# Performance work log

Measured on AMD Instinct MI355X. Metric: run time of the kernel, lower is better.

The kernel has to match this reference:

```python
import jax, jax.numpy as jnp
import numpy as np
from jax import lax

G = 64      # ngroup
CPN = 4     # channels per group in hidden layers
H, W = 32, 64
K = 5       # conv kernel
BIN = 8     # bin_num
BIAS = 3.5  # (bin_num-1)/2
NMIX = 3    # GMM components (batch replicas)
SCALE = 65536.0


def _group_mask(cout, cin, strict):
    # wavefront causality: tap (dg, di, dj) allowed iff dg+di+dj < 0 (strict) or <= 0
    g = jnp.arange(G)
    dg = g[None, :] - g[:, None]                      # (Gout, Gin)
    off = jnp.arange(K) - K // 2
    dd = off[:, None] + off[None, :]                  # (K, K)
    tot = dg[:, :, None, None] + dd[None, None, :, :]
    m = (tot < 0) if strict else (tot <= 0)
    m = jnp.repeat(jnp.repeat(m, cout, axis=0), cin, axis=1)
    return m.astype(jnp.float32)                      # (G*cout, G*cin, K, K)


def _cconv(x, w, b, m, relu):
    y = lax.conv_general_dilated(x, w * m, (1, 1), 'SAME',
                                 dimension_numbers=('NCHW', 'OIHW', 'NCHW'))
    y = y + b[None, :, None, None]
    return jax.nn.relu(y) if relu else y


def setup_inputs() -> dict:
    key = jax.random.key(0)
    ks = jax.random.split(key, 8)
    data = jax.random.randint(ks[0], (1, G, H, W), 0, BIN).astype(jnp.float32)
    mask = jax.random.randint(ks[1], (1, G, H, W), 0, 2).astype(jnp.float32)
    s = 0.05
    w_in = jax.random.normal(ks[2], (G * CPN, G, K, K), jnp.float32) * s
    b_in = jnp.zeros((G * CPN,), jnp.float32)
    w_hid = jax.random.normal(ks[3], (10, G * CPN, G * CPN, K, K), jnp.float32) * s
    b_hid = jnp.zeros((10, G * CPN), jnp.float32)
    w_out = jax.random.normal(ks[4], (G * NMIX, G * CPN, K, K), jnp.float32) * s
    b_out = jnp.zeros((G * NMIX,), jnp.float32)
    return dict(data=data, mask=mask, w_in=w_in, b_in=b_in,
                w_hid=w_hid, b_hid=b_hid, w_out=w_out, b_out=b_out)


def reference(data, mask, w_in, b_in, w_hid, b_hid, w_out, b_out):
    m_in = _group_mask(CPN, 1, True)      # first layer: strict (excludes current group)
    m_hid = _group_mask(CPN, CPN, False)
    m_out = _group_mask(NMIX, CPN, False)
    tdata = (data - BIAS) * mask
    x = jnp.concatenate([tdata, tdata, tdata], axis=0)   # (3, G, H, W)
    x = _cconv(x, w_in, b_in, m_in, True)
    for i in range(5):                                   # 5 residual blocks
        h = _cconv(x, w_hid[2 * i], b_hid[2 * i], m_hid, True)
        h = _cconv(h, w_hid[2 * i + 1], b_hid[2 * i + 1], m_hid, True)
        x = x + h
    y = _cconv(x, w_out, b_out, m_out, False)            # (3, G*3, H, W)
    y = y.reshape(NMIX, G, NMIX, H, W)                   # batch replica m -> mixture m
    logits = y[:, :, 0]
    mu = y[:, :, 1]
    sig = jax.nn.softplus(y[:, :, 2]) + 1e-6
    wts = jax.nn.softmax(logits, axis=0)                 # (3, G, H, W)
    edges = jnp.arange(BIN, dtype=jnp.float32) + 0.5 - BIAS
    z = (edges[:, None, None, None, None] - mu[None]) / (sig[None] * jnp.float32(np.sqrt(2.0)))
    cdf = 0.5 * (1.0 + lax.erf(z))                       # (BIN, 3, G, H, W)
    table = jnp.einsum('kmghw,mghw->ghwk', cdf, wts) * SCALE
    return table                                         # (G, H, W, BIN) quantizable CDF
```

## Files before the change

### kernel.cpp

```cpp
#include <hip/hip_runtime.h>
#include <math.h>

typedef _Float16 f16;
typedef _Float16 f16x8 __attribute__((ext_vector_type(8)));
typedef float f32x4 __attribute__((ext_vector_type(4)));

#define HH 32
#define WW 64
#define NPX 2048
#define SLOTS 68
#define LOSCALE 2048.0f
#define INV_LOSCALE 4.8828125e-4f

typedef const __attribute__((address_space(1))) void gvoid;
typedef __attribute__((address_space(3))) void lvoid;
__device__ __forceinline__ void gload_lds16(const void* g, void* l) {
    __builtin_amdgcn_global_load_lds((gvoid*)g, (lvoid*)l, 16, 0, 0);
}

__global__ void zero_kernel(f16* p, int n8) {
    int i = blockIdx.x * 256 + threadIdx.x;
    if (i < n8) *(int4*)(p + i * 8) = make_int4(0, 0, 0, 0);
}

__global__ void prep_kernel(const float* __restrict__ data,
                            const float* __restrict__ mask,
                            f16* __restrict__ X0, int plane) {
    int idx = blockIdx.x * 256 + threadIdx.x;
    if (idx >= NPX * 64) return;
    int px = idx >> 6, ci = idx & 63;
    int hh = px >> 6, w = px & 63;
    float v = (data[ci * NPX + px] - 3.5f) * mask[ci * NPX + px];
    int dst = ((hh + 2) * SLOTS + (w + 2)) * 64 + ci;
    X0[dst] = (f16)v;
    X0[plane + dst] = (f16)0.f;
}

__global__ void repack_kernel(const float* __restrict__ W, f16* __restrict__ WP,
                              int cin_log2, int coutp_log2,
                              int cpg_in_log2, int limb, int is_out) {
    int idx = blockIdx.x * 256 + threadIdx.x;
    int Cin = 1 << cin_log2;
    int plane = 25 << (cin_log2 + coutp_log2);
    int ci = idx & (Cin - 1);
    int rest = idx >> cin_log2;
    int co_p = rest & ((1 << coutp_log2) - 1);
    int tap = rest >> coutp_log2;
    if (tap >= 25) return;
    int ky = tap / 5, kx = tap - 5 * ky;
    int co_orig, g_out;
    if (is_out) { g_out = co_p >> 1; co_orig = 3 * g_out + 1 + (co_p & 1); }
    else        { g_out = co_p >> 2; co_orig = co_p; }
    int g_in = ci >> cpg_in_log2;
    float v = 0.f;
    if (ky + kx <= limb + g_out - g_in)
        v = W[(co_orig * Cin + ci) * 25 + tap];
    f16 vh = (f16)v;
    WP[idx] = vh;
    WP[plane + idx] = (f16)((v - (float)vh) * LOSCALE);
}

__global__ __launch_bounds__(320, 3) void conv_kernel(
    const f16* __restrict__ IN, int Cin, int inPlane,
    const f16* __restrict__ WP, int wPlane,
    const float* __restrict__ bias,
    const f16* __restrict__ RES, int resPlane,
    f16* __restrict__ OA, int oaPlane,
    float* __restrict__ OT,
    int nmt, int Coutp, int cpg_out, int cpg_in, int limb, int mode)
{
    __shared__ __align__(16) char SMEM[46080];
    f16* BL = (f16*)SMEM;
    float* RED = (float*)SMEM;

    const int t = threadIdx.x;
    const int kw = t >> 6;
    const int lane = t & 63, l15 = lane & 15, q = lane >> 4;

    int b = blockIdx.x;
    int half = nmt << 4;
    int slot = b >= half ? 1 : 0;
    int idx = b - (slot ? half : 0);
    int mt8 = idx >> 5;
    const int h = idx & 31;
    const int mt = slot ? (nmt - 1 - mt8) : mt8;
    const int co0 = mt * 16;
    const int g_max = (co0 + 15) / cpg_out;

    int cnt[5];
#pragma unroll
    for (int kx = 0; kx < 5; kx++) {
        int c = (g_max + limb - (kw + kx) + 1) * cpg_in;
        c = c < Cin ? c : Cin;
        cnt[kx] = c > 0 ? c : 0;
    }
    int ci_top = (g_max + limb + 1) * cpg_in;
    ci_top = ci_top < Cin ? ci_top : Cin;

    const f16* src[9];
#pragma unroll
    for (int r = 0; r < 9; r++) {
        int u = r * 320 + t;
        if (u >= 2720) u = 0;
        int plane = u / 1360;
        int rem = u - plane * 1360;
        int s4 = rem >> 2;
        int ci16 = rem & 3;
        int row = s4 / 68;
        int slt = s4 - row * 68;
        src[r] = IN + plane * inPlane + ((h + row) * SLOTS + slt) * Cin + ci16 * 8;
    }

    f32x4 acc_h[4], acc_m[4];
#pragma unroll
    for (int j = 0; j < 4; j++) {
        acc_h[j] = (f32x4){0.f, 0.f, 0.f, 0.f};
        acc_m[j] = (f32x4){0.f, 0.f, 0.f, 0.f};
    }

    const size_t kxs = (size_t)Coutp * Cin;

    for (int ci0 = 0; ci0 < ci_top; ci0 += 32) {
        __syncthreads();
#pragma unroll
        for (int r = 0; r < 9; r++) {
            int ub = r * 320 + kw * 64;
            if (ub < 2720)
                gload_lds16(src[r] + ci0, BL + ub * 8);
        }
        __syncthreads();

        const f16* wbase = WP + ((size_t)(kw * 5) * Coutp + co0) * Cin + ci0;
        f16x8 cah, cal, nah, nal;
        if (ci0 < cnt[0]) {
            cah = *(const f16x8*)(wbase + l15 * Cin + q * 8);
            cal = *(const f16x8*)(wbase + wPlane + l15 * Cin + q * 8);
        }
#pragma unroll
        for (int kx = 0; kx < 5; kx++) {
            if (ci0 >= cnt[kx]) break;
            if (kx < 4 && ci0 < cnt[kx + 1]) {
                nah = *(const f16x8*)(wbase + (kx + 1) * kxs + l15 * Cin + q * 8);
                nal = *(const f16x8*)(wbase + (kx + 1) * kxs + wPlane + l15 * Cin + q * 8);
            }
            f16x8 bh[4], bl[4];
#pragma unroll
            for (int j = 0; j < 4; j++) {
                int slt = j * 16 + l15 + kx;
                bh[j] = *(const f16x8*)&BL[(0 * 5 + kw) * (SLOTS * 32) + slt * 32 + q * 8];
                bl[j] = *(const f16x8*)&BL[(1 * 5 + kw) * (SLOTS * 32) + slt * 32 + q * 8];
            }
#pragma unroll
            for (int j = 0; j < 4; j++) {
                acc_h[j] = __builtin_amdgcn_mfma_f32_16x16x32_f16(cah, bh[j], acc_h[j], 0, 0, 0);
                acc_m[j] = __builtin_amdgcn_mfma_f32_16x16x32_f16(cah, bl[j], acc_m[j], 0, 0, 0);
                acc_m[j] = __builtin_amdgcn_mfma_f32_16x16x32_f16(cal, bh[j], acc_m[j], 0, 0, 0);
            }
            cah = nah; cal = nal;
        }
    }

    __syncthreads();
#pragma unroll
    for (int j = 0; j < 4; j++) {
        f32x4 v;
#pragma unroll
        for (int r = 0; r < 4; r++)
            v[r] = acc_h[j][r] + acc_m[j][r] * INV_LOSCALE;
        *(f32x4*)&RED[(kw * 64 + j * 16 + l15) * 20 + q * 4] = v;
    }
    __syncthreads();

    if (mode == 0) {
        for (int c = t; c < 1024; c += 320) {
            int px = c >> 4, col = c & 15;
            float v = bias[co0 + col];
#pragma unroll
            for (int k5 = 0; k5 < 5; k5++) v += RED[(k5 * 64 + px) * 20 + col];
            v = fmaxf(v, 0.f);
            int o = ((h + 2) * SLOTS + px + 2) * Coutp + co0 + col;
            if (RES) v += (float)RES[o] + (float)RES[resPlane + o] * INV_LOSCALE;
            f16 vh = (f16)v;
            OA[o] = vh;
            OA[oaPlane + o] = (f16)((v - (float)vh) * LOSCALE);
        }
    } else {
        for (int c = t; c < 1024; c += 320) {
            int px = c >> 4, col = c & 15;
            float v = bias[3 * ((co0 + col) >> 1) + 1 + (col & 1)];
#pragma unroll
            for (int k5 = 0; k5 < 5; k5++) v += RED[(k5 * 64 + px) * 20 + col];
            RED[px * 20 + col] = v;
        }
        __syncthreads();
        for (int c = t; c < 512; c += 320) {
            int px = c >> 3, gl = c & 7;
            float mu = RED[px * 20 + 2 * gl];
            float s  = RED[px * 20 + 2 * gl + 1];
            float sp = fmaxf(s, 0.f) + log1pf(expf(-fabsf(s)));
            float sig = sp + 1e-6f;
            float inv = 1.f / (sig * 1.41421356237f);
            int g = (co0 >> 1) + gl;
            float* o = OT + ((size_t)g * NPX + h * WW + px) * 8;
#pragma unroll
            for (int k = 0; k < 8; k++) {
                float z = ((float)k - 3.0f - mu) * inv;
                o[k] = 32768.f * (1.f + erff(z));
            }
        }
    }
}

extern "C" void kernel_launch(void* const* d_in, const int* in_sizes, int n_in,
                              void* d_out, int out_size, void* d_ws, size_t ws_size,
                              hipStream_t stream) {
    const float* data  = (const float*)d_in[0];
    const float* mask  = (const float*)d_in[1];
    const float* w_in  = (const float*)d_in[2];
    const float* b_in  = (const float*)d_in[3];
    const float* w_hid = (const float*)d_in[4];
    const float* b_hid = (const float*)d_in[5];
    const float* w_out = (const float*)d_in[6];
    const float* b_out = (const float*)d_in[7];
    float* out = (float*)d_out;

    f16* WP = (f16*)d_ws;
    f16* P  = WP + 3276800;
    f16* Q  = P + 1253376;
    f16* X0 = Q + 1253376;

    zero_kernel<<<1377, 256, 0, stream>>>(P, 352512);
    prep_kernel<<<512, 256, 0, stream>>>(data, mask, X0, 156672);

    repack_kernel<<<1600, 256, 0, stream>>>(w_in, WP, 6, 8, 0, 3, 0);
    conv_kernel<<<512, 320, 0, stream>>>(X0, 64, 156672, WP, 409600,
        b_in, nullptr, 0, P, 626688, nullptr, 16, 256, 4, 1, 3, 0);

    for (int i = 0; i < 5; i++) {
        repack_kernel<<<6400, 256, 0, stream>>>(w_hid + (size_t)(2 * i) * 1638400,
                                                WP, 8, 8, 2, 4, 0);
        conv_kernel<<<512, 320, 0, stream>>>(P, 256, 626688, WP, 1638400,
            b_hid + 2 * i * 256, nullptr, 0, Q, 626688, nullptr, 16, 256, 4, 4, 4, 0);
        repack_kernel<<<6400, 256, 0, stream>>>(w_hid + (size_t)(2 * i + 1) * 1638400,
                                                WP, 8, 8, 2, 4, 0);
        conv_kernel<<<512, 320, 0, stream>>>(Q, 256, 626688, WP, 1638400,
            b_hid + (2 * i + 1) * 256, P, 626688, P, 626688, nullptr, 16, 256, 4, 4, 4, 0);
    }

    repack_kernel<<<3200, 256, 0, stream>>>(w_out, WP, 8, 7, 2, 4, 1);
    conv_kernel<<<256, 320, 0, stream>>>(P, 256, 626688, WP, 819200,
        b_out, nullptr, 0, nullptr, 0, out, 8, 128, 2, 4, 4, 1);
}
```

Baseline: 497.3 us.

## Split conv tiles by half-width and batch all weight repacks into one launch

Each conv block now covers 32 output columns instead of 64. This halves the LDS footprint and doubles the grid, which lets launch bounds rise to 5 blocks per SM. All 12 weight repacks run as one 2D launch into separate workspace slices, replacing 12 interleaved repack launches between convs. The halo overhead per tile grows, since 36 slots are staged to produce 32 columns, and weight fragments are reloaded twice as often per output. Workspace use also grows by roughly 12x for the weights.

Result: slower. 583.0 us (+17.2%).

```diff
diff --git a/kernel.cpp b/kernel.cpp
--- a/kernel.cpp
+++ b/kernel.cpp
@@ -5,10 +5,8 @@
 typedef _Float16 f16x8 __attribute__((ext_vector_type(8)));
 typedef float f32x4 __attribute__((ext_vector_type(4)));
 
-#define HH 32
-#define WW 64
+#define SLOTS 68
 #define NPX 2048
-#define SLOTS 68
 #define LOSCALE 2048.0f
 #define INV_LOSCALE 4.8828125e-4f
 
@@ -36,12 +34,22 @@
     X0[plane + dst] = (f16)0.f;
 }
 
-__global__ void repack_kernel(const float* __restrict__ W, f16* __restrict__ WP,
-                              int cin_log2, int coutp_log2,
-                              int cpg_in_log2, int limb, int is_out) {
+__global__ void repack_all_kernel(const float* __restrict__ w_in,
+                                  const float* __restrict__ w_hid,
+                                  const float* __restrict__ w_out,
+                                  f16* __restrict__ WP) {
+    int layer = blockIdx.y;
     int idx = blockIdx.x * 256 + threadIdx.x;
+    int cin_log2   = (layer == 0) ? 6 : 8;
+    int coutp_log2 = (layer == 11) ? 7 : 8;
+    int cpg_in_log2 = (layer == 0) ? 0 : 2;
+    int limb = (layer == 0) ? 3 : 4;
+    int is_out = (layer == 11) ? 1 : 0;
+    const float* W = (layer == 0) ? w_in : (layer == 11) ? w_out
+                     : w_hid + (size_t)(layer - 1) * 1638400;
+    f16* WPl = WP + (size_t)layer * 3276800;
     int Cin = 1 << cin_log2;
-    int plane = 25 << (cin_log2 + coutp_log2);
+    int n = 25 << (cin_log2 + coutp_log2);
     int ci = idx & (Cin - 1);
     int rest = idx >> cin_log2;
     int co_p = rest & ((1 << coutp_log2) - 1);
@@ -56,11 +64,11 @@
     if (ky + kx <= limb + g_out - g_in)
         v = W[(co_orig * Cin + ci) * 25 + tap];
     f16 vh = (f16)v;
-    WP[idx] = vh;
-    WP[plane + idx] = (f16)((v - (float)vh) * LOSCALE);
-}
-
-__global__ __launch_bounds__(320, 3) void conv_kernel(
+    WPl[idx] = vh;
+    WPl[n + idx] = (f16)((v - (float)vh) * LOSCALE);
+}
+
+__global__ __launch_bounds__(320, 5) void conv_kernel(
     const f16* __restrict__ IN, int Cin, int inPlane,
     const f16* __restrict__ WP, int wPlane,
     const float* __restrict__ bias,
@@ -69,7 +77,7 @@
     float* __restrict__ OT,
     int nmt, int Coutp, int cpg_out, int cpg_in, int limb, int mode)
 {
-    __shared__ __align__(16) char SMEM[46080];
+    __shared__ __align__(16) char SMEM[23552];
     f16* BL = (f16*)SMEM;
     float* RED = (float*)SMEM;
 
@@ -78,12 +86,13 @@
     const int lane = t & 63, l15 = lane & 15, q = lane >> 4;
 
     int b = blockIdx.x;
-    int half = nmt << 4;
-    int slot = b >= half ? 1 : 0;
-    int idx = b - (slot ? half : 0);
-    int mt8 = idx >> 5;
-    const int h = idx & 31;
-    const int mt = slot ? (nmt - 1 - mt8) : mt8;
+    int half = nmt << 5;
+    int q2 = (b >= half) ? 1 : 0;
+    int r = b - (q2 ? half : 0);
+    int mt8 = r >> 5;
+    const int h = r & 31;
+    const int wx = q2;
+    const int mt = q2 ? (nmt - 1 - mt8) : mt8;
     const int co0 = mt * 16;
     const int g_max = (co0 + 15) / cpg_out;
 
@@ -97,23 +106,23 @@
     int ci_top = (g_max + limb + 1) * cpg_in;
     ci_top = ci_top < Cin ? ci_top : Cin;
 
-    const f16* src[9];
-#pragma unroll
-    for (int r = 0; r < 9; r++) {
-        int u = r * 320 + t;
-        if (u >= 2720) u = 0;
-        int plane = u / 1360;
-        int rem = u - plane * 1360;
+    const f16* src[5];
+#pragma unroll
+    for (int rr = 0; rr < 5; rr++) {
+        int u = rr * 320 + t;
+        if (u >= 1440) u = 0;
+        int plane = u / 720;
+        int rem = u - plane * 720;
         int s4 = rem >> 2;
-        int ci16 = rem & 3;
-        int row = s4 / 68;
-        int slt = s4 - row * 68;
-        src[r] = IN + plane * inPlane + ((h + row) * SLOTS + slt) * Cin + ci16 * 8;
-    }
-
-    f32x4 acc_h[4], acc_m[4];
-#pragma unroll
-    for (int j = 0; j < 4; j++) {
+        int c16 = rem & 3;
+        int row = s4 / 36;
+        int slot = s4 - row * 36;
+        src[rr] = IN + plane * inPlane + ((h + row) * SLOTS + wx * 32 + slot) * Cin + c16 * 8;
+    }
+
+    f32x4 acc_h[2], acc_m[2];
+#pragma unroll
+    for (int j = 0; j < 2; j++) {
         acc_h[j] = (f32x4){0.f, 0.f, 0.f, 0.f};
         acc_m[j] = (f32x4){0.f, 0.f, 0.f, 0.f};
     }
@@ -123,10 +132,10 @@
     for (int ci0 = 0; ci0 < ci_top; ci0 += 32) {
         __syncthreads();
 #pragma unroll
-        for (int r = 0; r < 9; r++) {
-            int ub = r * 320 + kw * 64;
-            if (ub < 2720)
-                gload_lds16(src[r] + ci0, BL + ub * 8);
+        for (int rr = 0; rr < 5; rr++) {
+            int ub = rr * 320 + kw * 64;
+            if (ub < 1440)
+                gload_lds16(src[rr] + ci0, BL + ub * 8);
         }
         __syncthreads();
 
@@ -143,15 +152,15 @@
                 nah = *(const f16x8*)(wbase + (kx + 1) * kxs + l15 * Cin + q * 8);
                 nal = *(const f16x8*)(wbase + (kx + 1) * kxs + wPlane + l15 * Cin + q * 8);
             }
-            f16x8 bh[4], bl[4];
-#pragma unroll
-            for (int j = 0; j < 4; j++) {
+            f16x8 bh[2], bl[2];
+#pragma unroll
+            for (int j = 0; j < 2; j++) {
                 int slt = j * 16 + l15 + kx;
-                bh[j] = *(const f16x8*)&BL[(0 * 5 + kw) * (SLOTS * 32) + slt * 32 + q * 8];
-                bl[j] = *(const f16x8*)&BL[(1 * 5 + kw) * (SLOTS * 32) + slt * 32 + q * 8];
-            }
-#pragma unroll
-            for (int j = 0; j < 4; j++) {
+                bh[j] = *(const f16x8*)&BL[((0 * 5 + kw) * 36 + slt) * 32 + q * 8];
+                bl[j] = *(const f16x8*)&BL[((1 * 5 + kw) * 36 + slt) * 32 + q * 8];
+            }
+#pragma unroll
+            for (int j = 0; j < 2; j++) {
                 acc_h[j] = __builtin_amdgcn_mfma_f32_16x16x32_f16(cah, bh[j], acc_h[j], 0, 0, 0);
                 acc_m[j] = __builtin_amdgcn_mfma_f32_16x16x32_f16(cah, bl[j], acc_m[j], 0, 0, 0);
                 acc_m[j] = __builtin_amdgcn_mfma_f32_16x16x32_f16(cal, bh[j], acc_m[j], 0, 0, 0);
@@ -162,38 +171,38 @@
 
     __syncthreads();
 #pragma unroll
-    for (int j = 0; j < 4; j++) {
+    for (int j = 0; j < 2; j++) {
         f32x4 v;
 #pragma unroll
-        for (int r = 0; r < 4; r++)
-            v[r] = acc_h[j][r] + acc_m[j][r] * INV_LOSCALE;
-        *(f32x4*)&RED[(kw * 64 + j * 16 + l15) * 20 + q * 4] = v;
+        for (int rr = 0; rr < 4; rr++)
+            v[rr] = acc_h[j][rr] + acc_m[j][rr] * INV_LOSCALE;
+        *(f32x4*)&RED[(kw * 32 + j * 16 + l15) * 20 + q * 4] = v;
     }
     __syncthreads();
 
     if (mode == 0) {
-        for (int c = t; c < 1024; c += 320) {
+        for (int c = t; c < 512; c += 320) {
             int px = c >> 4, col = c & 15;
             float v = bias[co0 + col];
 #pragma unroll
-            for (int k5 = 0; k5 < 5; k5++) v += RED[(k5 * 64 + px) * 20 + col];
+            for (int k5 = 0; k5 < 5; k5++) v += RED[(k5 * 32 + px) * 20 + col];
             v = fmaxf(v, 0.f);
-            int o = ((h + 2) * SLOTS + px + 2) * Coutp + co0 + col;
+            int o = ((h + 2) * SLOTS + wx * 32 + px + 2) * Coutp + co0 + col;
             if (RES) v += (float)RES[o] + (float)RES[resPlane + o] * INV_LOSCALE;
             f16 vh = (f16)v;
             OA[o] = vh;
             OA[oaPlane + o] = (f16)((v - (float)vh) * LOSCALE);
         }
     } else {
-        for (int c = t; c < 1024; c += 320) {
+        for (int c = t; c < 512; c += 320) {
             int px = c >> 4, col = c & 15;
             float v = bias[3 * ((co0 + col) >> 1) + 1 + (col & 1)];
 #pragma unroll
-            for (int k5 = 0; k5 < 5; k5++) v += RED[(k5 * 64 + px) * 20 + col];
+            for (int k5 = 0; k5 < 5; k5++) v += RED[(k5 * 32 + px) * 20 + col];
             RED[px * 20 + col] = v;
         }
         __syncthreads();
-        for (int c = t; c < 512; c += 320) {
+        for (int c = t; c < 256; c += 320) {
             int px = c >> 3, gl = c & 7;
             float mu = RED[px * 20 + 2 * gl];
             float s  = RED[px * 20 + 2 * gl + 1];
@@ -201,7 +210,7 @@
             float sig = sp + 1e-6f;
             float inv = 1.f / (sig * 1.41421356237f);
             int g = (co0 >> 1) + gl;
-            float* o = OT + ((size_t)g * NPX + h * WW + px) * 8;
+            float* o = OT + ((size_t)g * NPX + h * 64 + wx * 32 + px) * 8;
 #pragma unroll
             for (int k = 0; k < 8; k++) {
                 float z = ((float)k - 3.0f - mu) * inv;
@@ -225,29 +234,27 @@
     float* out = (float*)d_out;
 
     f16* WP = (f16*)d_ws;
-    f16* P  = WP + 3276800;
+    f16* P  = WP + (size_t)12 * 3276800;
     f16* Q  = P + 1253376;
     f16* X0 = Q + 1253376;
 
     zero_kernel<<<1377, 256, 0, stream>>>(P, 352512);
     prep_kernel<<<512, 256, 0, stream>>>(data, mask, X0, 156672);
-
-    repack_kernel<<<1600, 256, 0, stream>>>(w_in, WP, 6, 8, 0, 3, 0);
-    conv_kernel<<<512, 320, 0, stream>>>(X0, 64, 156672, WP, 409600,
+    repack_all_kernel<<<dim3(6400, 12), 256, 0, stream>>>(w_in, w_hid, w_out, WP);
+
+    conv_kernel<<<1024, 320, 0, stream>>>(X0, 64, 156672, WP, 409600,
         b_in, nullptr, 0, P, 626688, nullptr, 16, 256, 4, 1, 3, 0);
 
     for (int i = 0; i < 5; i++) {
-        repack_kernel<<<6400, 256, 0, stream>>>(w_hid + (size_t)(2 * i) * 1638400,
-                                                WP, 8, 8, 2, 4, 0);
-        conv_kernel<<<512, 320, 0, stream>>>(P, 256, 626688, WP, 1638400,
+        conv_kernel<<<1024, 320, 0, stream>>>(P, 256, 626688,
+            WP + (size_t)(1 + 2 * i) * 3276800, 1638400,
             b_hid + 2 * i * 256, nullptr, 0, Q, 626688, nullptr, 16, 256, 4, 4, 4, 0);
-        repack_kernel<<<6400, 256, 0, stream>>>(w_hid + (size_t)(2 * i + 1) * 1638400,
-                                                WP, 8, 8, 2, 4, 0);
-        conv_kernel<<<512, 320, 0, stream>>>(Q, 256, 626688, WP, 1638400,
+        conv_kernel<<<1024, 320, 0, stream>>>(Q, 256, 626688,
+            WP + (size_t)(2 + 2 * i) * 3276800, 1638400,
             b_hid + (2 * i + 1) * 256, P, 626688, P, 626688, nullptr, 16, 256, 4, 4, 4, 0);
     }
 
-    repack_kernel<<<3200, 256, 0, stream>>>(w_out, WP, 8, 7, 2, 4, 1);
-    conv_kernel<<<256, 320, 0, stream>>>(P, 256, 626688, WP, 819200,
+    conv_kernel<<<512, 320, 0, stream>>>(P, 256, 626688,
+        WP + (size_t)11 * 3276800, 819200,
         b_out, nullptr, 0, nullptr, 0, out, 8, 128, 2, 4, 4, 1);
 }
```
